# Kernel tuning notes

Hardware: AMD Instinct MI355X
Metric: run time of the kernel (lower is better)

## Reference

```python
import jax, jax.numpy as jnp
import numpy as np

D = 64          # d_in
NH = [256, 256] # nn_depth_design
L = 16          # flow_layers
B = 32768       # batch of samples


def _build_masks():
    # Deterministic mask maps: this_min=0, this_max=d_in-1 for all layers
    mh0 = np.arange(NH[0]) % (D - 1)
    mh1 = np.arange(NH[1]) % (D - 1)
    M1 = (mh0[None, :] <= mh1[:, None]).astype(np.float32)  # [nh1, nh0]
    M0s, M2s = [], []
    for l in range(L):
        perm = np.arange(D) if l % 2 == 0 else np.arange(D)[::-1]
        M0s.append((perm[None, :] <= mh0[:, None]).astype(np.float32))  # [nh0, D]
        M2s.append((mh1[None, :] < perm[:, None]).astype(np.float32))  # [D, nh1]
    M0 = np.stack(M0s)                                   # [L, nh0, D]
    M1 = np.broadcast_to(M1, (L,) + M1.shape).copy()     # [L, nh1, nh0]
    M2 = np.stack(M2s)                                   # [L, D, nh1]
    return jnp.asarray(M0), jnp.asarray(M1), jnp.asarray(M2)


def setup_inputs() -> dict:
    key = jax.random.key(0)
    ks = jax.random.split(key, 13)
    u = jax.random.normal(ks[0], (B, D), dtype=jnp.float32)

    def w(k, shape, fan_in):
        return jax.random.uniform(k, shape, jnp.float32, -1.0, 1.0) / np.sqrt(fan_in)

    inp = {"u": u}
    i = 1
    for net in ("loc", "scale"):
        inp[f"{net}_W0"] = w(ks[i], (L, NH[0], D), D); i += 1
        inp[f"{net}_b0"] = w(ks[i], (L, NH[0]), D); i += 1
        inp[f"{net}_W1"] = w(ks[i], (L, NH[1], NH[0]), NH[0]); i += 1
        inp[f"{net}_b1"] = w(ks[i], (L, NH[1]), NH[0]); i += 1
        inp[f"{net}_W2"] = w(ks[i], (L, D, NH[1]), NH[1]); i += 1
        inp[f"{net}_b2"] = w(ks[i], (L, D), NH[1]); i += 1
    M0, M1, M2 = _build_masks()
    inp["M0"], inp["M1"], inp["M2"] = M0, M1, M2
    return inp


def reference(u, loc_W0, loc_b0, loc_W1, loc_b1, loc_W2, loc_b2,
              scale_W0, scale_b0, scale_W1, scale_b1, scale_W2, scale_b2,
              M0, M1, M2):
    def step(y, p):
        (lW0, lb0, lW1, lb1, lW2, lb2,
         sW0, sb0, sW1, sb1, sW2, sb2, m0, m1, m2) = p

        def net(W0, b0, W1, b1, W2, b2):
            h = jax.nn.relu(y @ (m0 * W0).T + b0)    # [B, nh0]
            h = jax.nn.relu(h @ (m1 * W1).T + b1)    # [B, nh1]
            return h @ (m2 * W2).T + b2              # [B, D]

        loc = net(lW0, lb0, lW1, lb1, lW2, lb2)
        sc = net(sW0, sb0, sW1, sb1, sW2, sb2)
        # inverse=False coupling: exp(-scale) * (y - loc)
        return jnp.exp(-sc) * (y - loc), None

    params = (loc_W0, loc_b0, loc_W1, loc_b1, loc_W2, loc_b2,
              scale_W0, scale_b0, scale_W1, scale_b1, scale_W2, scale_b2,
              M0, M1, M2)
    y, _ = jax.lax.scan(step, u, params)
    return y
```

## Files before the change

### kernel.cpp

```cpp
#include <hip/hip_runtime.h>
#include <hip/hip_bf16.h>

typedef __bf16 bf16x8 __attribute__((ext_vector_type(8)));
typedef __bf16 bf16x4 __attribute__((ext_vector_type(4)));
typedef float  f32x4  __attribute__((ext_vector_type(4)));

#define LAYERS 16
#define DIM 64
#define NHID 256
#define BATCH 32768
#define MTILE 64
#define NBLOCKS (BATCH / MTILE)

#define W0P_PER 16384
#define W1P_PER 65536
#define W2P_PER 16384
#define W0P_TOT (32 * W0P_PER)
#define W1P_TOT (32 * W1P_PER)
#define W2P_TOT (32 * W2P_PER)
#define PACK_TOT (W0P_TOT + W1P_TOT + W2P_TOT)

__device__ __forceinline__ bf16x8 ldw(const __bf16* p) { return *(const bf16x8*)p; }

__global__ __launch_bounds__(256) void pack_weights(
    const float* __restrict__ lW0, const float* __restrict__ lW1, const float* __restrict__ lW2,
    const float* __restrict__ sW0, const float* __restrict__ sW1, const float* __restrict__ sW2,
    __bf16* __restrict__ ws)
{
    const long i = ((long)blockIdx.x * 256 + threadIdx.x) * 8;
    const float* W; long src; int l, n, k, which;
    if (i < W0P_TOT) {
        int netl = (int)(i / W0P_PER), rem = (int)(i % W0P_PER);
        int net = netl >> 4; l = netl & 15;
        int nt = rem >> 10, kt = (rem >> 9) & 1, lane = (rem >> 3) & 63;
        n = nt * 16 + (lane & 15); k = kt * 32 + (lane >> 4) * 8;
        W = net ? sW0 : lW0; which = 0;
        src = (long)(l * 256 + n) * 64 + k;
    } else if (i < W0P_TOT + W1P_TOT) {
        long r = i - W0P_TOT;
        int netl = (int)(r / W1P_PER), rem = (int)(r % W1P_PER);
        int net = netl >> 4; l = netl & 15;
        int nt = rem >> 12, kt = (rem >> 9) & 7, lane = (rem >> 3) & 63;
        n = nt * 16 + (lane & 15); k = kt * 32 + (lane >> 4) * 8;
        W = net ? sW1 : lW1; which = 1;
        src = (long)(l * 256 + n) * 256 + k;
    } else {
        long r = i - W0P_TOT - W1P_TOT;
        int netl = (int)(r / W2P_PER), rem = (int)(r % W2P_PER);
        int net = netl >> 4; l = netl & 15;
        int nt = rem >> 12, kt = (rem >> 9) & 7, lane = (rem >> 3) & 63;
        n = nt * 16 + (lane & 15); k = kt * 32 + (lane >> 4) * 8;
        W = net ? sW2 : lW2; which = 2;
        src = (long)(l * 64 + n) * 256 + k;
    }
    f32x4 wa = *(const f32x4*)(W + src);
    f32x4 wb = *(const f32x4*)(W + src + 4);
    const int nm = n % 63;
    const int pn = (l & 1) ? 63 - n : n;
    bf16x8 o;
    #pragma unroll
    for (int j = 0; j < 8; ++j) {
        int kk = k + j;
        bool m;
        if (which == 0)      { int pk = (l & 1) ? 63 - kk : kk; m = (pk <= nm); }
        else if (which == 1) { m = ((kk % 63) <= nm); }
        else                 { m = ((kk % 63) < pn); }
        float v = (j < 4) ? wa[j] : wb[j - 4];
        o[j] = m ? (__bf16)v : (__bf16)0.0f;
    }
    *(bf16x8*)(ws + i) = o;
}

__global__ void __launch_bounds__(256, 2)
flow_kernel(
    const float* __restrict__ u,
    const __bf16* __restrict__ wp,
    const float* __restrict__ lb0, const float* __restrict__ lb1, const float* __restrict__ lb2,
    const float* __restrict__ sb0, const float* __restrict__ sb1, const float* __restrict__ sb2,
    float* __restrict__ out)
{
    __shared__ __bf16 ybf[4 * 2 * 512];
    __shared__ __bf16 buf1[4 * 8 * 512];
    __shared__ __bf16 buf2[4 * 8 * 512];

    const int tid  = threadIdx.x;
    const int wave = tid >> 6;
    const int lane = tid & 63;
    const int quad = lane >> 4;
    const int l16  = lane & 15;
    const int blk  = blockIdx.x;

    const int qh = quad >> 1;
    const int qp = (quad & 1) * 4;

    const __bf16* w0p = wp;
    const __bf16* w1p = wp + W0P_TOT;
    const __bf16* w2p = wp + W0P_TOT + W1P_TOT;

    f32x4 y[4];
    #pragma unroll
    for (int bt = 0; bt < 4; ++bt)
        y[bt] = *(const f32x4*)(u + (long)(blk * MTILE + bt * 16 + l16) * DIM
                                  + wave * 16 + quad * 4);

    const int ktY = wave >> 1;
    const int flY = ((wave & 1) * 2 + qh) * 16 + l16;

    bf16x8 wg1[8];
    #pragma unroll
    for (int ot = 0; ot < 4; ++ot)
        #pragma unroll
        for (int kt = 0; kt < 2; ++kt)
            wg1[ot * 2 + kt] = ldw(w0p + (long)((4 * wave + ot) * 2 + kt) * 512 + lane * 8);

    for (int l = 0; l < LAYERS; ++l) {
        #pragma unroll
        for (int bt = 0; bt < 4; ++bt) {
            bf16x4 v;
            #pragma unroll
            for (int r = 0; r < 4; ++r) v[r] = (__bf16)y[bt][r];
            *(bf16x4*)&ybf[((bt * 2 + ktY) * 64 + flY) * 8 + qp] = v;
        }
        __syncthreads();

        f32x4 locr[4], scr[4];

        #pragma unroll
        for (int net = 0; net < 2; ++net) {
            const __bf16* w1b = w1p + (long)(net * 16 + l) * W1P_PER;
            const __bf16* w2b = w2p + (long)(net * 16 + l) * W2P_PER;
            const __bf16* w0n = w0p + (long)(net == 0 ? 16 + l : l + 1) * W0P_PER;
            const float* b0 = (net ? sb0 : lb0) + l * 256;
            const float* b1 = (net ? sb1 : lb1) + l * 256;
            const float* b2 = (net ? sb2 : lb2) + l * 64;

            bf16x8 wg2a[16];

            {
                f32x4 acc[4][4];
                #pragma unroll
                for (int ot = 0; ot < 4; ++ot)
                    #pragma unroll
                    for (int bt = 0; bt < 4; ++bt)
                        acc[ot][bt] = (f32x4){0.f, 0.f, 0.f, 0.f};
                #pragma unroll
                for (int kt = 0; kt < 2; ++kt) {
                    bf16x8 bv[4];
                    #pragma unroll
                    for (int bt = 0; bt < 4; ++bt)
                        bv[bt] = *(const bf16x8*)&ybf[((bt * 2 + kt) * 64 + lane) * 8];
                    #pragma unroll
                    for (int ot = 0; ot < 4; ++ot)
                        #pragma unroll
                        for (int bt = 0; bt < 4; ++bt)
                            acc[ot][bt] = __builtin_amdgcn_mfma_f32_16x16x32_bf16(wg1[ot * 2 + kt], bv[bt], acc[ot][bt], 0, 0, 0);
                }
                #pragma unroll
                for (int kt = 0; kt < 4; ++kt)
                    #pragma unroll
                    for (int ot = 0; ot < 4; ++ot)
                        wg2a[kt * 4 + ot] = ldw(w1b + (long)((4 * wave + ot) * 8 + kt) * 512 + lane * 8);
                #pragma unroll
                for (int ot = 0; ot < 4; ++ot) {
                    f32x4 bias = *(const f32x4*)(b0 + (4 * wave + ot) * 16 + quad * 4);
                    const int kt1 = (4 * wave + ot) >> 1;
                    const int fl  = ((ot & 1) * 2 + qh) * 16 + l16;
                    #pragma unroll
                    for (int bt = 0; bt < 4; ++bt) {
                        bf16x4 v;
                        #pragma unroll
                        for (int r = 0; r < 4; ++r)
                            v[r] = (__bf16)fmaxf(acc[ot][bt][r] + bias[r], 0.f);
                        *(bf16x4*)&buf1[((bt * 8 + kt1) * 64 + fl) * 8 + qp] = v;
                    }
                }
            }
            __syncthreads();

            bf16x8 wg3[8];

            {
                f32x4 acc[4][4];
                #pragma unroll
                for (int ot = 0; ot < 4; ++ot)
                    #pragma unroll
                    for (int bt = 0; bt < 4; ++bt)
                        acc[ot][bt] = (f32x4){0.f, 0.f, 0.f, 0.f};
                #pragma unroll
                for (int kt = 0; kt < 8; ++kt) {
                    bf16x8 aw[4];
                    #pragma unroll
                    for (int ot = 0; ot < 4; ++ot)
                        aw[ot] = (kt < 4) ? wg2a[kt * 4 + ot]
                                          : ldw(w1b + (long)((4 * wave + ot) * 8 + kt) * 512 + lane * 8);
                    bf16x8 bv[4];
                    #pragma unroll
                    for (int bt = 0; bt < 4; ++bt)
                        bv[bt] = *(const bf16x8*)&buf1[((bt * 8 + kt) * 64 + lane) * 8];
                    #pragma unroll
                    for (int ot = 0; ot < 4; ++ot)
                        #pragma unroll
                        for (int bt = 0; bt < 4; ++bt)
                            acc[ot][bt] = __builtin_amdgcn_mfma_f32_16x16x32_bf16(aw[ot], bv[bt], acc[ot][bt], 0, 0, 0);
                }
                #pragma unroll
                for (int ot = 0; ot < 4; ++ot) {
                    f32x4 bias = *(const f32x4*)(b1 + (4 * wave + ot) * 16 + quad * 4);
                    const int kt1 = (4 * wave + ot) >> 1;
                    const int fl  = ((ot & 1) * 2 + qh) * 16 + l16;
                    #pragma unroll
                    for (int bt = 0; bt < 4; ++bt) {
                        bf16x4 v;
                        #pragma unroll
                        for (int r = 0; r < 4; ++r)
                            v[r] = (__bf16)fmaxf(acc[ot][bt][r] + bias[r], 0.f);
                        *(bf16x4*)&buf2[((bt * 8 + kt1) * 64 + fl) * 8 + qp] = v;
                    }
                }
                #pragma unroll
                for (int kt = 0; kt < 8; ++kt)
                    wg3[kt] = ldw(w2b + (long)(wave * 8 + kt) * 512 + lane * 8);
            }
            __syncthreads();

            {
                f32x4 acc[4];
                #pragma unroll
                for (int bt = 0; bt < 4; ++bt)
                    acc[bt] = (f32x4){0.f, 0.f, 0.f, 0.f};
                #pragma unroll
                for (int kt = 0; kt < 8; ++kt) {
                    #pragma unroll
                    for (int bt = 0; bt < 4; ++bt) {
                        bf16x8 bv = *(const bf16x8*)&buf2[((bt * 8 + kt) * 64 + lane) * 8];
                        acc[bt] = __builtin_amdgcn_mfma_f32_16x16x32_bf16(wg3[kt], bv, acc[bt], 0, 0, 0);
                    }
                }
                #pragma unroll
                for (int ot = 0; ot < 4; ++ot)
                    #pragma unroll
                    for (int kt = 0; kt < 2; ++kt)
                        wg1[ot * 2 + kt] = ldw(w0n + (long)((4 * wave + ot) * 2 + kt) * 512 + lane * 8);
                f32x4 bias = *(const f32x4*)(b2 + wave * 16 + quad * 4);
                if (net == 0) {
                    #pragma unroll
                    for (int bt = 0; bt < 4; ++bt)
                        #pragma unroll
                        for (int r = 0; r < 4; ++r)
                            locr[bt][r] = acc[bt][r] + bias[r];
                } else {
                    #pragma unroll
                    for (int bt = 0; bt < 4; ++bt)
                        #pragma unroll
                        for (int r = 0; r < 4; ++r)
                            scr[bt][r] = acc[bt][r] + bias[r];
                }
            }
        }

        #pragma unroll
        for (int bt = 0; bt < 4; ++bt)
            #pragma unroll
            for (int r = 0; r < 4; ++r)
                y[bt][r] = __expf(-scr[bt][r]) * (y[bt][r] - locr[bt][r]);
    }

    #pragma unroll
    for (int bt = 0; bt < 4; ++bt)
        *(f32x4*)(out + (long)(blk * MTILE + bt * 16 + l16) * DIM
                      + wave * 16 + quad * 4) = y[bt];
}

extern "C" void kernel_launch(void* const* d_in, const int* in_sizes, int n_in,
                              void* d_out, int out_size, void* d_ws, size_t ws_size,
                              hipStream_t stream) {
    const float* u   = (const float*)d_in[0];
    const float* lW0 = (const float*)d_in[1];
    const float* lb0 = (const float*)d_in[2];
    const float* lW1 = (const float*)d_in[3];
    const float* lb1 = (const float*)d_in[4];
    const float* lW2 = (const float*)d_in[5];
    const float* lb2 = (const float*)d_in[6];
    const float* sW0 = (const float*)d_in[7];
    const float* sb0 = (const float*)d_in[8];
    const float* sW1 = (const float*)d_in[9];
    const float* sb1 = (const float*)d_in[10];
    const float* sW2 = (const float*)d_in[11];
    const float* sb2 = (const float*)d_in[12];

    if (ws_size < (size_t)PACK_TOT * sizeof(__bf16)) return;
    __bf16* ws = (__bf16*)d_ws;

    pack_weights<<<PACK_TOT / 8 / 256, 256, 0, stream>>>(
        lW0, lW1, lW2, sW0, sW1, sW2, ws);
    flow_kernel<<<NBLOCKS, 256, 0, stream>>>(
        u, ws, lb0, lb1, lb2, sb0, sb1, sb2, (float*)d_out);
}
```

Baseline: 314.5 us.

## Share one LDS activation buffer and shrink weight prefetch to raise occupancy

The two hidden-activation LDS buffers are merged into one, and extra barriers are added so the buffer can be reused safely between layer stages and across the two nets. Register-held weight prefetch arrays shrink (wg2a from 16 to 4, wg3 from 8 to 4) and launch bounds go from 2 to 4 blocks per CU, to cut LDS and VGPR use per block and allow more resident waves. The cost is two extra __syncthreads per net and more weight loads issued inside the MFMA loops instead of being prefetched. Whether the added occupancy hides that latency is uncertain.

```diff
diff --git a/kernel.cpp b/kernel.cpp
--- a/kernel.cpp
+++ b/kernel.cpp
@@ -71,7 +71,7 @@
     *(bf16x8*)(ws + i) = o;
 }
 
-__global__ void __launch_bounds__(256, 2)
+__global__ void __launch_bounds__(256, 4)
 flow_kernel(
     const float* __restrict__ u,
     const __bf16* __restrict__ wp,
@@ -80,8 +80,7 @@
     float* __restrict__ out)
 {
     __shared__ __bf16 ybf[4 * 2 * 512];
-    __shared__ __bf16 buf1[4 * 8 * 512];
-    __shared__ __bf16 buf2[4 * 8 * 512];
+    __shared__ __bf16 buf[4 * 8 * 512];
 
     const int tid  = threadIdx.x;
     const int wave = tid >> 6;
@@ -134,7 +133,7 @@
             const float* b1 = (net ? sb1 : lb1) + l * 256;
             const float* b2 = (net ? sb2 : lb2) + l * 64;
 
-            bf16x8 wg2a[16];
+            bf16x8 wg2a[4];
 
             {
                 f32x4 acc[4][4];
@@ -156,10 +155,8 @@
                             acc[ot][bt] = __builtin_amdgcn_mfma_f32_16x16x32_bf16(wg1[ot * 2 + kt], bv[bt], acc[ot][bt], 0, 0, 0);
                 }
                 #pragma unroll
-                for (int kt = 0; kt < 4; ++kt)
-                    #pragma unroll
-                    for (int ot = 0; ot < 4; ++ot)
-                        wg2a[kt * 4 + ot] = ldw(w1b + (long)((4 * wave + ot) * 8 + kt) * 512 + lane * 8);
+                for (int ot = 0; ot < 4; ++ot)
+                    wg2a[ot] = ldw(w1b + (long)((4 * wave + ot) * 8 + 0) * 512 + lane * 8);
                 #pragma unroll
                 for (int ot = 0; ot < 4; ++ot) {
                     f32x4 bias = *(const f32x4*)(b0 + (4 * wave + ot) * 16 + quad * 4);
@@ -171,38 +168,45 @@
                         #pragma unroll
                         for (int r = 0; r < 4; ++r)
                             v[r] = (__bf16)fmaxf(acc[ot][bt][r] + bias[r], 0.f);
-                        *(bf16x4*)&buf1[((bt * 8 + kt1) * 64 + fl) * 8 + qp] = v;
+                        *(bf16x4*)&buf[((bt * 8 + kt1) * 64 + fl) * 8 + qp] = v;
                     }
                 }
             }
             __syncthreads();
 
-            bf16x8 wg3[8];
-
+            bf16x8 wg3[4];
+
+            f32x4 acc2[4][4];
             {
-                f32x4 acc[4][4];
                 #pragma unroll
                 for (int ot = 0; ot < 4; ++ot)
                     #pragma unroll
                     for (int bt = 0; bt < 4; ++bt)
-                        acc[ot][bt] = (f32x4){0.f, 0.f, 0.f, 0.f};
+                        acc2[ot][bt] = (f32x4){0.f, 0.f, 0.f, 0.f};
                 #pragma unroll
                 for (int kt = 0; kt < 8; ++kt) {
                     bf16x8 aw[4];
                     #pragma unroll
                     for (int ot = 0; ot < 4; ++ot)
-                        aw[ot] = (kt < 4) ? wg2a[kt * 4 + ot]
+                        aw[ot] = (kt < 1) ? wg2a[ot]
                                           : ldw(w1b + (long)((4 * wave + ot) * 8 + kt) * 512 + lane * 8);
                     bf16x8 bv[4];
                     #pragma unroll
                     for (int bt = 0; bt < 4; ++bt)
-                        bv[bt] = *(const bf16x8*)&buf1[((bt * 8 + kt) * 64 + lane) * 8];
+                        bv[bt] = *(const bf16x8*)&buf[((bt * 8 + kt) * 64 + lane) * 8];
                     #pragma unroll
                     for (int ot = 0; ot < 4; ++ot)
                         #pragma unroll
                         for (int bt = 0; bt < 4; ++bt)
-                            acc[ot][bt] = __builtin_amdgcn_mfma_f32_16x16x32_bf16(aw[ot], bv[bt], acc[ot][bt], 0, 0, 0);
-                }
+                            acc2[ot][bt] = __builtin_amdgcn_mfma_f32_16x16x32_bf16(aw[ot], bv[bt], acc2[ot][bt], 0, 0, 0);
+                }
+                #pragma unroll
+                for (int kt = 0; kt < 4; ++kt)
+                    wg3[kt] = ldw(w2b + (long)(wave * 8 + kt) * 512 + lane * 8);
+            }
+            __syncthreads();
+
+            {
                 #pragma unroll
                 for (int ot = 0; ot < 4; ++ot) {
                     f32x4 bias = *(const f32x4*)(b1 + (4 * wave + ot) * 16 + quad * 4);
@@ -213,13 +217,10 @@
                         bf16x4 v;
                         #pragma unroll
                         for (int r = 0; r < 4; ++r)
-                            v[r] = (__bf16)fmaxf(acc[ot][bt][r] + bias[r], 0.f);
-                        *(bf16x4*)&buf2[((bt * 8 + kt1) * 64 + fl) * 8 + qp] = v;
+                            v[r] = (__bf16)fmaxf(acc2[ot][bt][r] + bias[r], 0.f);
+                        *(bf16x4*)&buf[((bt * 8 + kt1) * 64 + fl) * 8 + qp] = v;
                     }
                 }
-                #pragma unroll
-                for (int kt = 0; kt < 8; ++kt)
-                    wg3[kt] = ldw(w2b + (long)(wave * 8 + kt) * 512 + lane * 8);
             }
             __syncthreads();
 
@@ -230,10 +231,12 @@
                     acc[bt] = (f32x4){0.f, 0.f, 0.f, 0.f};
                 #pragma unroll
                 for (int kt = 0; kt < 8; ++kt) {
+                    bf16x8 aw = (kt < 4) ? wg3[kt]
+                                         : ldw(w2b + (long)(wave * 8 + kt) * 512 + lane * 8);
                     #pragma unroll
                     for (int bt = 0; bt < 4; ++bt) {
-                        bf16x8 bv = *(const bf16x8*)&buf2[((bt * 8 + kt) * 64 + lane) * 8];
-                        acc[bt] = __builtin_amdgcn_mfma_f32_16x16x32_bf16(wg3[kt], bv, acc[bt], 0, 0, 0);
+                        bf16x8 bv = *(const bf16x8*)&buf[((bt * 8 + kt) * 64 + lane) * 8];
+                        acc[bt] = __builtin_amdgcn_mfma_f32_16x16x32_bf16(aw, bv, acc[bt], 0, 0, 0);
                     }
                 }
                 #pragma unroll
@@ -256,6 +259,7 @@
                             scr[bt][r] = acc[bt][r] + bias[r];
                 }
             }
+            if (net == 0) __syncthreads();
         }
 
         #pragma unroll
```

After: 514.3 us. +63.5%, slower.

## Double batch tile to 128 rows with 8 waves splitting output features

Applied to the files above, without the earlier changes.

Doubles the batch rows per block to 128 and the threads per block to 512 (8 waves). Each wave now owns 2 output tiles across all 8 batch tiles, instead of 4 output tiles across 4 batch tiles. Each block streams the same weights as before over twice as many rows, which halves total weight traffic from global/L2, and register use per wave drops. In exchange each block needs twice the LDS, the grid has half as many blocks, and the layer-2 per-wave weight prefetch gets shallower.

```diff
diff --git a/kernel.cpp b/kernel.cpp
--- a/kernel.cpp
+++ b/kernel.cpp
@@ -9,7 +9,7 @@
 #define DIM 64
 #define NHID 256
 #define BATCH 32768
-#define MTILE 64
+#define MTILE 128
 #define NBLOCKS (BATCH / MTILE)
 
 #define W0P_PER 16384
@@ -71,7 +71,7 @@
     *(bf16x8*)(ws + i) = o;
 }
 
-__global__ void __launch_bounds__(256, 2)
+__global__ void __launch_bounds__(512, 2)
 flow_kernel(
     const float* __restrict__ u,
     const __bf16* __restrict__ wp,
@@ -79,9 +79,9 @@
     const float* __restrict__ sb0, const float* __restrict__ sb1, const float* __restrict__ sb2,
     float* __restrict__ out)
 {
-    __shared__ __bf16 ybf[4 * 2 * 512];
-    __shared__ __bf16 buf1[4 * 8 * 512];
-    __shared__ __bf16 buf2[4 * 8 * 512];
+    __shared__ __bf16 ybf[8 * 2 * 512];
+    __shared__ __bf16 buf1[8 * 8 * 512];
+    __shared__ __bf16 buf2[8 * 8 * 512];
 
     const int tid  = threadIdx.x;
     const int wave = tid >> 6;
@@ -93,33 +93,37 @@
     const int qh = quad >> 1;
     const int qp = (quad & 1) * 4;
 
+    const int ob = 2 * wave;
+    const int d  = wave >> 1;
+    const int hb = (wave & 1) * 4;
+
     const __bf16* w0p = wp;
     const __bf16* w1p = wp + W0P_TOT;
     const __bf16* w2p = wp + W0P_TOT + W1P_TOT;
 
     f32x4 y[4];
     #pragma unroll
-    for (int bt = 0; bt < 4; ++bt)
-        y[bt] = *(const f32x4*)(u + (long)(blk * MTILE + bt * 16 + l16) * DIM
-                                  + wave * 16 + quad * 4);
-
-    const int ktY = wave >> 1;
-    const int flY = ((wave & 1) * 2 + qh) * 16 + l16;
-
-    bf16x8 wg1[8];
+    for (int j = 0; j < 4; ++j)
+        y[j] = *(const f32x4*)(u + (long)(blk * MTILE + (hb + j) * 16 + l16) * DIM
+                                 + d * 16 + quad * 4);
+
+    const int ktY = d >> 1;
+    const int flY = ((d & 1) * 2 + qh) * 16 + l16;
+
+    bf16x8 wg1[4];
     #pragma unroll
-    for (int ot = 0; ot < 4; ++ot)
+    for (int ot = 0; ot < 2; ++ot)
         #pragma unroll
         for (int kt = 0; kt < 2; ++kt)
-            wg1[ot * 2 + kt] = ldw(w0p + (long)((4 * wave + ot) * 2 + kt) * 512 + lane * 8);
+            wg1[ot * 2 + kt] = ldw(w0p + (long)((ob + ot) * 2 + kt) * 512 + lane * 8);
 
     for (int l = 0; l < LAYERS; ++l) {
         #pragma unroll
-        for (int bt = 0; bt < 4; ++bt) {
+        for (int j = 0; j < 4; ++j) {
             bf16x4 v;
             #pragma unroll
-            for (int r = 0; r < 4; ++r) v[r] = (__bf16)y[bt][r];
-            *(bf16x4*)&ybf[((bt * 2 + ktY) * 64 + flY) * 8 + qp] = v;
+            for (int r = 0; r < 4; ++r) v[r] = (__bf16)y[j][r];
+            *(bf16x4*)&ybf[(((hb + j) * 2 + ktY) * 64 + flY) * 8 + qp] = v;
         }
         __syncthreads();
 
@@ -134,39 +138,38 @@
             const float* b1 = (net ? sb1 : lb1) + l * 256;
             const float* b2 = (net ? sb2 : lb2) + l * 64;
 
-            bf16x8 wg2a[16];
+            bf16x8 wg2a[4];
 
             {
-                f32x4 acc[4][4];
-                #pragma unroll
-                for (int ot = 0; ot < 4; ++ot)
-                    #pragma unroll
-                    for (int bt = 0; bt < 4; ++bt)
+                f32x4 acc[2][8];
+                #pragma unroll
+                for (int ot = 0; ot < 2; ++ot)
+                    #pragma unroll
+                    for (int bt = 0; bt < 8; ++bt)
                         acc[ot][bt] = (f32x4){0.f, 0.f, 0.f, 0.f};
                 #pragma unroll
                 for (int kt = 0; kt < 2; ++kt) {
-                    bf16x8 bv[4];
-                    #pragma unroll
-                    for (int bt = 0; bt < 4; ++bt)
-                        bv[bt] = *(const bf16x8*)&ybf[((bt * 2 + kt) * 64 + lane) * 8];
-                    #pragma unroll
-                    for (int ot = 0; ot < 4; ++ot)
-                        #pragma unroll
-                        for (int bt = 0; bt < 4; ++bt)
-                            acc[ot][bt] = __builtin_amdgcn_mfma_f32_16x16x32_bf16(wg1[ot * 2 + kt], bv[bt], acc[ot][bt], 0, 0, 0);
-                }
-                #pragma unroll
-                for (int kt = 0; kt < 4; ++kt)
-                    #pragma unroll
-                    for (int ot = 0; ot < 4; ++ot)
-                        wg2a[kt * 4 + ot] = ldw(w1b + (long)((4 * wave + ot) * 8 + kt) * 512 + lane * 8);
-                #pragma unroll
-                for (int ot = 0; ot < 4; ++ot) {
-                    f32x4 bias = *(const f32x4*)(b0 + (4 * wave + ot) * 16 + quad * 4);
-                    const int kt1 = (4 * wave + ot) >> 1;
-                    const int fl  = ((ot & 1) * 2 + qh) * 16 + l16;
-                    #pragma unroll
-                    for (int bt = 0; bt < 4; ++bt) {
+                    #pragma unroll
+                    for (int bt = 0; bt < 8; ++bt) {
+                        bf16x8 bv = *(const bf16x8*)&ybf[((bt * 2 + kt) * 64 + lane) * 8];
+                        #pragma unroll
+                        for (int ot = 0; ot < 2; ++ot)
+                            acc[ot][bt] = __builtin_amdgcn_mfma_f32_16x16x32_bf16(wg1[ot * 2 + kt], bv, acc[ot][bt], 0, 0, 0);
+                    }
+                }
+                #pragma unroll
+                for (int kt = 0; kt < 2; ++kt)
+                    #pragma unroll
+                    for (int ot = 0; ot < 2; ++ot)
+                        wg2a[kt * 2 + ot] = ldw(w1b + (long)((ob + ot) * 8 + kt) * 512 + lane * 8);
+                #pragma unroll
+                for (int ot = 0; ot < 2; ++ot) {
+                    const int o = ob + ot;
+                    f32x4 bias = *(const f32x4*)(b0 + o * 16 + quad * 4);
+                    const int kt1 = o >> 1;
+                    const int fl  = ((o & 1) * 2 + qh) * 16 + l16;
+                    #pragma unroll
+                    for (int bt = 0; bt < 8; ++bt) {
                         bf16x4 v;
                         #pragma unroll
                         for (int r = 0; r < 4; ++r)
@@ -177,39 +180,38 @@
             }
             __syncthreads();
 
-            bf16x8 wg3[8];
+            bf16x8 wg3[2];
 
             {
-                f32x4 acc[4][4];
-                #pragma unroll
-                for (int ot = 0; ot < 4; ++ot)
-                    #pragma unroll
-                    for (int bt = 0; bt < 4; ++bt)
+                f32x4 acc[2][8];
+                #pragma unroll
+                for (int ot = 0; ot < 2; ++ot)
+                    #pragma unroll
+                    for (int bt = 0; bt < 8; ++bt)
                         acc[ot][bt] = (f32x4){0.f, 0.f, 0.f, 0.f};
                 #pragma unroll
                 for (int kt = 0; kt < 8; ++kt) {
-                    bf16x8 aw[4];
-                    #pragma unroll
-                    for (int ot = 0; ot < 4; ++ot)
-                        aw[ot] = (kt < 4) ? wg2a[kt * 4 + ot]
-                                          : ldw(w1b + (long)((4 * wave + ot) * 8 + kt) * 512 + lane * 8);
-                    bf16x8 bv[4];
-                    #pragma unroll
-                    for (int bt = 0; bt < 4; ++bt)
-                        bv[bt] = *(const bf16x8*)&buf1[((bt * 8 + kt) * 64 + lane) * 8];
-                    #pragma unroll
-                    for (int ot = 0; ot < 4; ++ot)
-                        #pragma unroll
-                        for (int bt = 0; bt < 4; ++bt)
-                            acc[ot][bt] = __builtin_amdgcn_mfma_f32_16x16x32_bf16(aw[ot], bv[bt], acc[ot][bt], 0, 0, 0);
-                }
-                #pragma unroll
-                for (int ot = 0; ot < 4; ++ot) {
-                    f32x4 bias = *(const f32x4*)(b1 + (4 * wave + ot) * 16 + quad * 4);
-                    const int kt1 = (4 * wave + ot) >> 1;
-                    const int fl  = ((ot & 1) * 2 + qh) * 16 + l16;
-                    #pragma unroll
-                    for (int bt = 0; bt < 4; ++bt) {
+                    bf16x8 aw[2];
+                    #pragma unroll
+                    for (int ot = 0; ot < 2; ++ot)
+                        aw[ot] = (kt < 2) ? wg2a[kt * 2 + ot]
+                                          : ldw(w1b + (long)((ob + ot) * 8 + kt) * 512 + lane * 8);
+                    #pragma unroll
+                    for (int bt = 0; bt < 8; ++bt) {
+                        bf16x8 bv = *(const bf16x8*)&buf1[((bt * 8 + kt) * 64 + lane) * 8];
+                        #pragma unroll
+                        for (int ot = 0; ot < 2; ++ot)
+                            acc[ot][bt] = __builtin_amdgcn_mfma_f32_16x16x32_bf16(aw[ot], bv, acc[ot][bt], 0, 0, 0);
+                    }
+                }
+                #pragma unroll
+                for (int ot = 0; ot < 2; ++ot) {
+                    const int o = ob + ot;
+                    f32x4 bias = *(const f32x4*)(b1 + o * 16 + quad * 4);
+                    const int kt1 = o >> 1;
+                    const int fl  = ((o & 1) * 2 + qh) * 16 + l16;
+                    #pragma unroll
+                    for (int bt = 0; bt < 8; ++bt) {
                         bf16x4 v;
                         #pragma unroll
                         for (int r = 0; r < 4; ++r)
@@ -218,57 +220,59 @@
                     }
                 }
                 #pragma unroll
-                for (int kt = 0; kt < 8; ++kt)
-                    wg3[kt] = ldw(w2b + (long)(wave * 8 + kt) * 512 + lane * 8);
+                for (int kt = 0; kt < 2; ++kt)
+                    wg3[kt] = ldw(w2b + (long)(d * 8 + kt) * 512 + lane * 8);
             }
             __syncthreads();
 
             {
                 f32x4 acc[4];
                 #pragma unroll
-                for (int bt = 0; bt < 4; ++bt)
-                    acc[bt] = (f32x4){0.f, 0.f, 0.f, 0.f};
+                for (int j = 0; j < 4; ++j)
+                    acc[j] = (f32x4){0.f, 0.f, 0.f, 0.f};
                 #pragma unroll
                 for (int kt = 0; kt < 8; ++kt) {
-                    #pragma unroll
-                    for (int bt = 0; bt < 4; ++bt) {
-                        bf16x8 bv = *(const bf16x8*)&buf2[((bt * 8 + kt) * 64 + lane) * 8];
-                        acc[bt] = __builtin_amdgcn_mfma_f32_16x16x32_bf16(wg3[kt], bv, acc[bt], 0, 0, 0);
-                    }
-                }
-                #pragma unroll
-                for (int ot = 0; ot < 4; ++ot)
+                    bf16x8 aw = (kt < 2) ? wg3[kt]
+                                         : ldw(w2b + (long)(d * 8 + kt) * 512 + lane * 8);
+                    #pragma unroll
+                    for (int j = 0; j < 4; ++j) {
+                        bf16x8 bv = *(const bf16x8*)&buf2[(((hb + j) * 8 + kt) * 64 + lane) * 8];
+                        acc[j] = __builtin_amdgcn_mfma_f32_16x16x32_bf16(aw, bv, acc[j], 0, 0, 0);
+                    }
+                }
+                #pragma unroll
+                for (int ot = 0; ot < 2; ++ot)
                     #pragma unroll
                     for (int kt = 0; kt < 2; ++kt)
-                        wg1[ot * 2 + kt] = ldw(w0n + (long)((4 * wave + ot) * 2 + kt) * 512 + lane * 8);
-                f32x4 bias = *(const f32x4*)(b2 + wave * 16 + quad * 4);
+                        wg1[ot * 2 + kt] = ldw(w0n + (long)((ob + ot) * 2 + kt) * 512 + lane * 8);
+                f32x4 bias = *(const f32x4*)(b2 + d * 16 + quad * 4);
                 if (net == 0) {
                     #pragma unroll
-                    for (int bt = 0; bt < 4; ++bt)
+                    for (int j = 0; j < 4; ++j)
                         #pragma unroll
                         for (int r = 0; r < 4; ++r)
-                            locr[bt][r] = acc[bt][r] + bias[r];
+                            locr[j][r] = acc[j][r] + bias[r];
                 } else {
                     #pragma unroll
-                    for (int bt = 0; bt < 4; ++bt)
+                    for (int j = 0; j < 4; ++j)
                         #pragma unroll
                         for (int r = 0; r < 4; ++r)
-                            scr[bt][r] = acc[bt][r] + bias[r];
+                            scr[j][r] = acc[j][r] + bias[r];
                 }
             }
         }
 
         #pragma unroll
-        for (int bt = 0; bt < 4; ++bt)
+        for (int j = 0; j < 4; ++j)
             #pragma unroll
             for (int r = 0; r < 4; ++r)
-                y[bt][r] = __expf(-scr[bt][r]) * (y[bt][r] - locr[bt][r]);
+                y[j][r] = __expf(-scr[j][r]) * (y[j][r] - locr[j][r]);
     }
 
     #pragma unroll
-    for (int bt = 0; bt < 4; ++bt)
-        *(f32x4*)(out + (long)(blk * MTILE + bt * 16 + l16) * DIM
-                      + wave * 16 + quad * 4) = y[bt];
+    for (int j = 0; j < 4; ++j)
+        *(f32x4*)(out + (long)(blk * MTILE + (hb + j) * 16 + l16) * DIM
+                      + d * 16 + quad * 4) = y[j];
 }
 
 extern "C" void kernel_launch(void* const* d_in, const int* in_sizes, int n_in,
@@ -293,6 +297,6 @@
 
     pack_weights<<<PACK_TOT / 8 / 256, 256, 0, stream>>>(
         lW0, lW1, lW2, sW0, sW1, sW2, ws);
-    flow_kernel<<<NBLOCKS, 256, 0, stream>>>(
+    flow_kernel<<<NBLOCKS, 512, 0, stream>>>(
         u, ws, lb0, lb1, lb2, sb0, sb1, sb2, (float*)d_out);
 }
```

Measured after the change: 382.2 us. +21.5%, slower.
